# Performance work log

Measured on AMD Instinct MI355X. Metric: run time of the kernel, lower is better.

Reference implementation:

```python
import jax, jax.numpy as jnp
import numpy as np

B, S, D = 2, 2048, 1024
H, DQK, DV = 16, 64, 64
DECAY = 0.85


def _fractal_weights(seq_len: int, decay: float) -> np.ndarray:
    # Dragon-curve hierarchical weights: earlier (coarser) positions get higher
    # weight; weight decays by `decay` per hierarchy level. Normalized to sum 1,
    # matching DragonCurveGenerator.get_hierarchical_weights semantics.
    idx = np.arange(seq_len)
    level = np.floor(np.log2(idx + 1)).astype(np.int32)
    w = decay ** level.astype(np.float32)
    return (w / w.sum()).astype(np.float32)


def setup_inputs() -> dict:
    key = jax.random.key(0)
    kx, kq, kk, kv, ko = jax.random.split(key, 5)
    s = 1.0 / np.sqrt(D)
    return {
        "x": jax.random.normal(kx, (B, S, D), dtype=jnp.float32),
        "Wq": jax.random.normal(kq, (D, H * DQK), dtype=jnp.float32) * s,
        "Wk": jax.random.normal(kk, (D, H * DQK), dtype=jnp.float32) * s,
        "Wv": jax.random.normal(kv, (D, H * DV), dtype=jnp.float32) * s,
        "Wo": jax.random.normal(ko, (H * DV, D), dtype=jnp.float32) * s,
        "fractal_weights": jnp.asarray(_fractal_weights(S, DECAY)),
    }


def reference(x, Wq, Wk, Wv, Wo, fractal_weights):
    b, s, _ = x.shape
    # Projections (Linear with bias=False); weights stored as (in, out).
    Q = (x @ Wq).reshape(b, s, H, DQK).transpose(0, 2, 1, 3)  # [B,H,S,Dqk]
    K = (x @ Wk).reshape(b, s, H, DQK).transpose(0, 2, 1, 3)
    V = (x @ Wv).reshape(b, s, H, DV).transpose(0, 2, 1, 3)   # [B,H,S,Dv]
    scale = 1.0 / jnp.sqrt(jnp.asarray(DQK, dtype=x.dtype))
    scores = jnp.einsum("bhqd,bhkd->bhqk", Q, K) * scale      # [B,H,S,S]
    # Multiplicative per-key fractal bias applied BEFORE softmax.
    scores = scores * fractal_weights[None, None, None, :]
    attn = jax.nn.softmax(scores, axis=-1)
    out = jnp.einsum("bhqk,bhkd->bhqd", attn, V)               # [B,H,S,Dv]
    out = out.transpose(0, 2, 1, 3).reshape(b, s, H * DV)
    return out @ Wo                                            # [B,S,D]
```

## Files before the change

### kernel.cpp

```cpp
#include <hip/hip_runtime.h>
#include <hip/hip_bf16.h>
#include <stdint.h>

#define B_  2
#define S_  2048
#define D_  1024
#define H_  16
#define DH_ 64

typedef __attribute__((ext_vector_type(8))) __bf16    bf16x8;
typedef __attribute__((ext_vector_type(8))) _Float16  f16x8;
typedef __attribute__((ext_vector_type(4))) _Float16  f16x4;
typedef __attribute__((ext_vector_type(2))) __fp16    fp16x2;
typedef __attribute__((ext_vector_type(4))) float     f32x4;

__device__ inline unsigned short f2bf(float f) {
    union { float f; uint32_t u; } v; v.f = f;
    uint32_t r = (v.u + 0x7fffu + ((v.u >> 16) & 1u)) >> 16;
    return (unsigned short)r;
}

__device__ __forceinline__ void g2l16(const unsigned short* g, unsigned short* l) {
    __builtin_amdgcn_global_load_lds(
        (const __attribute__((address_space(1))) unsigned int*)g,
        (__attribute__((address_space(3))) unsigned int*)l,
        16, 0, 0);
}


__global__ void convert_x(const float* __restrict__ x, unsigned short* __restrict__ xb, int n) {
    int i = (blockIdx.x * blockDim.x + threadIdx.x) * 4;
    if (i < n) {
        float4 v = *(const float4*)(x + i);
        ushort4 o;
        o.x = f2bf(v.x); o.y = f2bf(v.y); o.z = f2bf(v.z); o.w = f2bf(v.w);
        *(ushort4*)(xb + i) = o;
    }
}

__global__ void transpose_w(const float* __restrict__ s0, const float* __restrict__ s1,
                            const float* __restrict__ s2, const float* __restrict__ s3,
                            unsigned short* __restrict__ d0, unsigned short* __restrict__ d1,
                            unsigned short* __restrict__ d2, unsigned short* __restrict__ d3) {
    __shared__ float tile[32][33];
    const float* src; unsigned short* dst;
    switch (blockIdx.z) {
        case 0: src = s0; dst = d0; break;
        case 1: src = s1; dst = d1; break;
        case 2: src = s2; dst = d2; break;
        default: src = s3; dst = d3; break;
    }
    int n0 = blockIdx.x * 32, k0 = blockIdx.y * 32;
    int tx = threadIdx.x, ty = threadIdx.y;
    for (int j = 0; j < 32; j += 8)
        tile[ty + j][tx] = src[(long)(k0 + ty + j) * 1024 + n0 + tx];
    __syncthreads();
    for (int j = 0; j < 32; j += 8)
        dst[(long)(n0 + ty + j) * 1024 + k0 + tx] = f2bf(tile[tx][ty + j]);
}

__global__ __launch_bounds__(256, 2)
void gemm128(const unsigned short* __restrict__ A, const unsigned short* __restrict__ Bt,
             unsigned short* __restrict__ Qo, unsigned short* __restrict__ Ko,
             unsigned short* __restrict__ Vt,
             const float* __restrict__ fw)
{
    __shared__ __align__(16) unsigned short As[128 * 64];
    __shared__ __align__(16) unsigned short Bs[128 * 64];
    const int tid  = threadIdx.x;
    const int lane = tid & 63, wid = tid >> 6;
    const int quad = lane >> 4, l15 = lane & 15;
    const int wm = wid >> 1, wn = wid & 1;
    const int bm = blockIdx.y, bn = blockIdx.x;
    const int K = 1024;
    f32x4 acc[4][4] = {};
    const long Abase = (long)bm * 128 * K;
    const long Bbase = (long)bn * 128 * K;

    for (int k0 = 0; k0 < K; k0 += 64) {
        __syncthreads();
#pragma unroll
        for (int i = 0; i < 4; i++) {
            int slot = i * 256 + wid * 64 + lane;
            int row = slot >> 3, cp = slot & 7;
            int c = cp ^ (row & 7);
            g2l16(A + Abase + (long)row * K + k0 + c * 8, &As[(i * 256 + wid * 64) * 8]);
        }
#pragma unroll
        for (int i = 0; i < 4; i++) {
            int slot = i * 256 + wid * 64 + lane;
            int row = slot >> 3, cp = slot & 7;
            int c = cp ^ (row & 7);
            g2l16(Bt + Bbase + (long)row * K + k0 + c * 8, &Bs[(i * 256 + wid * 64) * 8]);
        }
        __syncthreads();
#pragma unroll
        for (int ks = 0; ks < 2; ks++) {
            bf16x8 af[4], bfr[4];
#pragma unroll
            for (int t = 0; t < 4; t++) {
                int ra = wm * 64 + t * 16 + l15;
                af[t]  = *(const bf16x8*)(As + ra * 64 + (((ks * 4 + quad) ^ (l15 & 7))) * 8);
                int rb = wn * 64 + t * 16 + l15;
                bfr[t] = *(const bf16x8*)(Bs + rb * 64 + (((ks * 4 + quad) ^ (l15 & 7))) * 8);
            }
#pragma unroll
            for (int tm = 0; tm < 4; tm++)
#pragma unroll
                for (int tn = 0; tn < 4; tn++)
                    acc[tm][tn] = __builtin_amdgcn_mfma_f32_16x16x32_bf16(af[tm], bfr[tn], acc[tm][tn], 0, 0, 0);
        }
    }

    const float Cq = 0.125f * 1.44269504f;
    for (int tm = 0; tm < 4; tm++)
        for (int tn = 0; tn < 4; tn++)
            for (int r = 0; r < 4; r++) {
                int gm = bm * 128 + wm * 64 + tm * 16 + quad * 4 + r;
                int gn = bn * 128 + wn * 64 + tn * 16 + l15;
                float v = acc[tm][tn][r];
                int b = gm >> 11, s = gm & 2047;
                if (gn < 1024) {
                    int h = gn >> 6, d = gn & 63;
                    Qo[(((long)(b * H_ + h) * S_ + s) << 6) + d] = f2bf(v * Cq);
                } else if (gn < 2048) {
                    int g = gn - 1024; int h = g >> 6, d = g & 63;
                    Ko[(((long)(b * H_ + h) * S_ + s) << 6) + d] = f2bf(v * fw[s]);
                } else {
                    int g = gn - 2048; int h = g >> 6, d = g & 63;
                    union { _Float16 h; unsigned short u; } cv;
                    cv.h = (_Float16)v;
                    int sp = s ^ ((d & 8) ? 4 : 0);
                    Vt[((long)(b * H_ + h) * DH_ + d) * S_ + sp] = cv.u;
                }
            }
}

__global__ __launch_bounds__(256, 4)
void gemm_wo(const unsigned short* __restrict__ A, const unsigned short* __restrict__ Bt,
             float* __restrict__ Cout)
{
    __shared__ __align__(16) unsigned short As[64 * 64];
    __shared__ __align__(16) unsigned short Bs[64 * 64];
    const int tid  = threadIdx.x;
    const int lane = tid & 63, wid = tid >> 6;
    const int quad = lane >> 4, l15 = lane & 15;
    const int bm = blockIdx.y, bn = blockIdx.x;
    const int K = 1024;
    f32x4 acc[4] = {};
    const long Abase = (long)bm * 64 * K;
    const long Bbase = (long)bn * 64 * K;

    for (int k0 = 0; k0 < K; k0 += 64) {
        __syncthreads();
#pragma unroll
        for (int i = 0; i < 2; i++) {
            int base = i * 256 + wid * 64;
            int slot = base + lane;
            int row = slot >> 3, cp = slot & 7;
            int c = cp ^ (row & 7);
            g2l16(A + Abase + (long)row * K + k0 + c * 8, &As[base * 8]);
        }
#pragma unroll
        for (int i = 0; i < 2; i++) {
            int base = i * 256 + wid * 64;
            int slot = base + lane;
            int row = slot >> 3, cp = slot & 7;
            int c = cp ^ (row & 7);
            g2l16(Bt + Bbase + (long)row * K + k0 + c * 8, &Bs[base * 8]);
        }
        __syncthreads();
#pragma unroll
        for (int ks = 0; ks < 2; ks++) {
            bf16x8 af, bfr[4];
            {
                int ra = wid * 16 + l15;
                af = *(const bf16x8*)(As + ra * 64 + (((ks * 4 + quad) ^ (l15 & 7))) * 8);
            }
#pragma unroll
            for (int tt = 0; tt < 4; tt++) {
                int rb = tt * 16 + l15;
                bfr[tt] = *(const bf16x8*)(Bs + rb * 64 + (((ks * 4 + quad) ^ (l15 & 7))) * 8);
            }
#pragma unroll
            for (int tn = 0; tn < 4; tn++)
                acc[tn] = __builtin_amdgcn_mfma_f32_16x16x32_bf16(af, bfr[tn], acc[tn], 0, 0, 0);
        }
    }

    for (int tn = 0; tn < 4; tn++)
        for (int r = 0; r < 4; r++) {
            int gm = bm * 64 + wid * 16 + quad * 4 + r;
            int gn = bn * 64 + tn * 16 + l15;
            Cout[(long)gm * 1024 + gn] = acc[tn][r];
        }
}

__global__ __launch_bounds__(512, 2)
void attn_kernel(const unsigned short* __restrict__ Q, const unsigned short* __restrict__ Kb,
                 const unsigned short* __restrict__ Vt,
                 unsigned short* __restrict__ O)
{
    __shared__ __align__(16) unsigned short smem[2][2][2][64 * 64];

    const int tid  = threadIdx.x;
    const int lane = tid & 63, wid = tid >> 6;
    const int half = wid >> 2, sw = wid & 3;
    const int quad = lane >> 4, l15 = lane & 15;
    const int bh = blockIdx.y;
    const int qt = blockIdx.x;

    const unsigned short* Kg = Kb + (long)bh * S_ * DH_;
    const unsigned short* Vg = Vt + (long)bh * (long)DH_ * S_;

    bf16x8 qf[4][2];
#pragma unroll
    for (int st = 0; st < 4; st++) {
        const unsigned short* Qp = Q + ((long)bh * S_ + qt * 256 + sw * 64 + st * 16 + l15) * DH_ + quad * 8;
        qf[st][0] = *(const bf16x8*)(Qp);
        qf[st][1] = *(const bf16x8*)(Qp + 32);
    }

    auto issue = [&](int buf, int kt) {
#pragma unroll
        for (int i = 0; i < 2; i++) {
            int base = i * 256 + sw * 64;
            int slot = base + lane;
            int row = slot >> 3, cp = slot & 7;
            int c = cp ^ (row & 7);
            g2l16(Kg + ((long)(kt * 64 + row) * 64 + c * 8), &smem[half][buf][0][base * 8]);
        }
#pragma unroll
        for (int i = 0; i < 2; i++) {
            int base = i * 256 + sw * 64;
            int slot = base + lane;
            int row = slot >> 3, cp = slot & 7;
            int c = cp ^ (row & 7);
            g2l16(Vg + ((long)row * S_ + kt * 64 + c * 8), &smem[half][buf][1][base * 8]);
        }
    };

    f32x4 oacc[4][4] = {};
    f32x4 lacc[4] = {};
    const f16x8 vone = {(_Float16)1.f, (_Float16)1.f, (_Float16)1.f, (_Float16)1.f,
                        (_Float16)1.f, (_Float16)1.f, (_Float16)1.f, (_Float16)1.f};

    const int kt0 = half * 16;
    issue(0, kt0);
    __syncthreads();

    const int hf = (((quad & 1) ^ ((l15 >> 3) & 1))) * 4;

    for (int t = 0; t < 16; t++) {
        const int cur = t & 1;
        if (t + 1 < 16) issue(1 - cur, kt0 + t + 1);

        const unsigned short* Kc = &smem[half][cur][0][0];
        const unsigned short* Vc = &smem[half][cur][1][0];

        f32x4 sacc[4][4] = {};
#pragma unroll
        for (int kc = 0; kc < 4; kc++) {
            int row = kc * 16 + l15;
            bf16x8 k0 = *(const bf16x8*)(Kc + (row * 8 + (quad       ^ (l15 & 7))) * 8);
            bf16x8 k1 = *(const bf16x8*)(Kc + (row * 8 + ((4 + quad) ^ (l15 & 7))) * 8);
#pragma unroll
            for (int st = 0; st < 4; st++) {
                sacc[st][kc] = __builtin_amdgcn_mfma_f32_16x16x32_bf16(k0, qf[st][0], sacc[st][kc], 0, 0, 0);
                sacc[st][kc] = __builtin_amdgcn_mfma_f32_16x16x32_bf16(k1, qf[st][1], sacc[st][kc], 0, 0, 0);
            }
        }

        f16x8 vfr[2][4];
#pragma unroll
        for (int c = 0; c < 2; c++)
#pragma unroll
            for (int dt = 0; dt < 4; dt++) {
                int row = dt * 16 + l15;
                int p0 = (c * 4 +     (quad >> 1)) ^ (l15 & 7);
                int p1 = (c * 4 + 2 + (quad >> 1)) ^ (l15 & 7);
                f16x4 v0 = *(const f16x4*)(Vc + row * 64 + p0 * 8 + hf);
                f16x4 v1 = *(const f16x4*)(Vc + row * 64 + p1 * 8 + hf);
                vfr[c][dt] = __builtin_shufflevector(v0, v1, 0, 1, 2, 3, 4, 5, 6, 7);
            }

        f16x8 pk8[4][2];
#pragma unroll
        for (int st = 0; st < 4; st++)
#pragma unroll
            for (int c = 0; c < 2; c++) {
                union { uint4 u; f16x8 v; } pku;
#pragma unroll
                for (int hh = 0; hh < 2; hh++) {
                    float p0 = __builtin_amdgcn_exp2f(sacc[st][2 * c + hh][0]);
                    float p1 = __builtin_amdgcn_exp2f(sacc[st][2 * c + hh][1]);
                    float p2 = __builtin_amdgcn_exp2f(sacc[st][2 * c + hh][2]);
                    float p3 = __builtin_amdgcn_exp2f(sacc[st][2 * c + hh][3]);
                    union { fp16x2 h2; unsigned int u; } a, b;
                    a.h2 = __builtin_amdgcn_cvt_pkrtz(p0, p1);
                    b.h2 = __builtin_amdgcn_cvt_pkrtz(p2, p3);
                    if (hh == 0) { pku.u.x = a.u; pku.u.y = b.u; }
                    else         { pku.u.z = a.u; pku.u.w = b.u; }
                }
                pk8[st][c] = pku.v;
            }

#pragma unroll
        for (int c = 0; c < 2; c++) {
#pragma unroll
            for (int st = 0; st < 4; st++)
                lacc[st] = __builtin_amdgcn_mfma_f32_16x16x32_f16(pk8[st][c], vone, lacc[st], 0, 0, 0);
#pragma unroll
            for (int dt = 0; dt < 4; dt++)
#pragma unroll
                for (int st = 0; st < 4; st++)
                    oacc[st][dt] = __builtin_amdgcn_mfma_f32_16x16x32_f16(pk8[st][c], vfr[c][dt], oacc[st][dt], 0, 0, 0);
        }

        __syncthreads();
    }

    float* ov = (float*)&smem[0][0][0][0];
    float* lv = ov + 128 * 66;
    int b = bh >> 4, h = bh & 15;

#pragma unroll
    for (int p = 0; p < 2; p++) {
        if (half == 1) {
#pragma unroll
            for (int si = 0; si < 2; si++) {
                int st = 2 * p + si;
#pragma unroll
                for (int dt = 0; dt < 4; dt++)
#pragma unroll
                    for (int r = 0; r < 4; r++) {
                        int qr = sw * 32 + si * 16 + quad * 4 + r;
                        ov[qr * 66 + dt * 16 + l15] = oacc[st][dt][r];
                    }
                if (l15 == 0) {
#pragma unroll
                    for (int r = 0; r < 4; r++)
                        lv[sw * 32 + si * 16 + quad * 4 + r] = lacc[st][r];
                }
            }
        }
        __syncthreads();
        if (half == 0) {
#pragma unroll
            for (int si = 0; si < 2; si++) {
                int st = 2 * p + si;
#pragma unroll
                for (int r = 0; r < 4; r++) {
                    int qr = sw * 32 + si * 16 + quad * 4 + r;
                    float inv = 1.0f / (lacc[st][r] + lv[qr]);
                    int srow = qt * 256 + sw * 64 + st * 16 + quad * 4 + r;
#pragma unroll
                    for (int dt = 0; dt < 4; dt++) {
                        float val = oacc[st][dt][r] + ov[qr * 66 + dt * 16 + l15];
                        O[((long)(b * S_ + srow)) * 1024 + h * DH_ + dt * 16 + l15] = f2bf(val * inv);
                    }
                }
            }
        }
        __syncthreads();
    }
}


extern "C" void kernel_launch(void* const* d_in, const int* in_sizes, int n_in,
                              void* d_out, int out_size, void* d_ws, size_t ws_size,
                              hipStream_t stream)
{
    const float* x  = (const float*)d_in[0];
    const float* Wq = (const float*)d_in[1];
    const float* Wk = (const float*)d_in[2];
    const float* Wv = (const float*)d_in[3];
    const float* Wo = (const float*)d_in[4];
    const float* fw = (const float*)d_in[5];
    float* out = (float*)d_out;

    char* ws = (char*)d_ws;
    unsigned short* xb    = (unsigned short*)(ws);
    unsigned short* WqkvT = (unsigned short*)(ws + 8388608);
    unsigned short* WoT   = (unsigned short*)(ws + 14680064);
    unsigned short* Qb    = (unsigned short*)(ws + 16777216);
    unsigned short* Kb    = (unsigned short*)(ws + 25165824);
    unsigned short* Vt    = (unsigned short*)(ws + 33554432);
    unsigned short* Ob    = xb;

    convert_x<<<dim3((B_ * S_ * D_) / 4 / 256), dim3(256), 0, stream>>>(x, xb, B_ * S_ * D_);
    transpose_w<<<dim3(32, 32, 4), dim3(32, 8), 0, stream>>>(
        Wq, Wk, Wv, Wo,
        WqkvT, WqkvT + 1024 * 1024, WqkvT + 2 * 1024 * 1024, WoT);
    gemm128<<<dim3(24, 32), dim3(256), 0, stream>>>(xb, WqkvT, Qb, Kb, Vt, fw);
    attn_kernel<<<dim3(S_ / 256, B_ * H_), dim3(512), 0, stream>>>(Qb, Kb, Vt, Ob);
    gemm_wo<<<dim3(16, 64), dim3(256), 0, stream>>>(Ob, WoT, out);
}
```

Measured before the change: 180.1 us.

## Split QKV GEMM K-loop across 8 waves and fuse prep kernels

The QKV projection GEMM now runs 512 threads per block: two groups of four waves each take one half of every 64-wide K slice, and their partial accumulators are reduced through shared memory in the epilogue before the scatter to Q/K/Vt. This is meant to raise wave-level parallelism and latency hiding in the main GEMM, at the cost of a shared-memory reduction with extra barriers. Separately, the x conversion and the weight transpose are merged into one launch to save kernel launch overhead. Register pressure under the new 512,4 launch bounds could force spills.

```diff
diff --git a/kernel.cpp b/kernel.cpp
--- a/kernel.cpp
+++ b/kernel.cpp
@@ -27,50 +27,55 @@
         16, 0, 0);
 }
 
-
-__global__ void convert_x(const float* __restrict__ x, unsigned short* __restrict__ xb, int n) {
-    int i = (blockIdx.x * blockDim.x + threadIdx.x) * 4;
-    if (i < n) {
+__global__ void prep(const float* __restrict__ x, unsigned short* __restrict__ xb,
+                     const float* __restrict__ s0, const float* __restrict__ s1,
+                     const float* __restrict__ s2, const float* __restrict__ s3,
+                     unsigned short* __restrict__ d0, unsigned short* __restrict__ d1,
+                     unsigned short* __restrict__ d2, unsigned short* __restrict__ d3)
+{
+    __shared__ float tile[32][33];
+    int bid = blockIdx.x, tid = threadIdx.x;
+    if (bid < 4096) {
+        int i = (bid * 256 + tid) * 4;
         float4 v = *(const float4*)(x + i);
         ushort4 o;
         o.x = f2bf(v.x); o.y = f2bf(v.y); o.z = f2bf(v.z); o.w = f2bf(v.w);
         *(ushort4*)(xb + i) = o;
-    }
-}
-
-__global__ void transpose_w(const float* __restrict__ s0, const float* __restrict__ s1,
-                            const float* __restrict__ s2, const float* __restrict__ s3,
-                            unsigned short* __restrict__ d0, unsigned short* __restrict__ d1,
-                            unsigned short* __restrict__ d2, unsigned short* __restrict__ d3) {
-    __shared__ float tile[32][33];
-    const float* src; unsigned short* dst;
-    switch (blockIdx.z) {
-        case 0: src = s0; dst = d0; break;
-        case 1: src = s1; dst = d1; break;
-        case 2: src = s2; dst = d2; break;
-        default: src = s3; dst = d3; break;
-    }
-    int n0 = blockIdx.x * 32, k0 = blockIdx.y * 32;
-    int tx = threadIdx.x, ty = threadIdx.y;
-    for (int j = 0; j < 32; j += 8)
-        tile[ty + j][tx] = src[(long)(k0 + ty + j) * 1024 + n0 + tx];
-    __syncthreads();
-    for (int j = 0; j < 32; j += 8)
-        dst[(long)(n0 + ty + j) * 1024 + k0 + tx] = f2bf(tile[tx][ty + j]);
-}
-
-__global__ __launch_bounds__(256, 2)
+    } else {
+        int tb = bid - 4096;
+        int z = tb >> 10, t = tb & 1023;
+        int bx = t & 31, by = t >> 5;
+        const float* src; unsigned short* dst;
+        switch (z) {
+            case 0: src = s0; dst = d0; break;
+            case 1: src = s1; dst = d1; break;
+            case 2: src = s2; dst = d2; break;
+            default: src = s3; dst = d3; break;
+        }
+        int n0 = bx * 32, k0 = by * 32;
+        int tx = tid & 31, ty = tid >> 5;
+        for (int j = 0; j < 32; j += 8)
+            tile[ty + j][tx] = src[(long)(k0 + ty + j) * 1024 + n0 + tx];
+        __syncthreads();
+        for (int j = 0; j < 32; j += 8)
+            dst[(long)(n0 + ty + j) * 1024 + k0 + tx] = f2bf(tile[tx][ty + j]);
+    }
+}
+
+__global__ __launch_bounds__(512, 4)
 void gemm128(const unsigned short* __restrict__ A, const unsigned short* __restrict__ Bt,
              unsigned short* __restrict__ Qo, unsigned short* __restrict__ Ko,
              unsigned short* __restrict__ Vt,
              const float* __restrict__ fw)
 {
-    __shared__ __align__(16) unsigned short As[128 * 64];
-    __shared__ __align__(16) unsigned short Bs[128 * 64];
+    __shared__ __align__(16) unsigned short Smem[2][128 * 64];
+    unsigned short* As = &Smem[0][0];
+    unsigned short* Bs = &Smem[1][0];
     const int tid  = threadIdx.x;
     const int lane = tid & 63, wid = tid >> 6;
     const int quad = lane >> 4, l15 = lane & 15;
-    const int wm = wid >> 1, wn = wid & 1;
+    const int ks   = wid >> 2;
+    const int wm   = (wid >> 1) & 1, wn = wid & 1;
     const int bm = blockIdx.y, bn = blockIdx.x;
     const int K = 1024;
     f32x4 acc[4][4] = {};
@@ -80,60 +85,79 @@
     for (int k0 = 0; k0 < K; k0 += 64) {
         __syncthreads();
 #pragma unroll
-        for (int i = 0; i < 4; i++) {
-            int slot = i * 256 + wid * 64 + lane;
-            int row = slot >> 3, cp = slot & 7;
-            int c = cp ^ (row & 7);
-            g2l16(A + Abase + (long)row * K + k0 + c * 8, &As[(i * 256 + wid * 64) * 8]);
-        }
-#pragma unroll
-        for (int i = 0; i < 4; i++) {
-            int slot = i * 256 + wid * 64 + lane;
-            int row = slot >> 3, cp = slot & 7;
-            int c = cp ^ (row & 7);
-            g2l16(Bt + Bbase + (long)row * K + k0 + c * 8, &Bs[(i * 256 + wid * 64) * 8]);
-        }
-        __syncthreads();
-#pragma unroll
-        for (int ks = 0; ks < 2; ks++) {
-            bf16x8 af[4], bfr[4];
-#pragma unroll
-            for (int t = 0; t < 4; t++) {
-                int ra = wm * 64 + t * 16 + l15;
-                af[t]  = *(const bf16x8*)(As + ra * 64 + (((ks * 4 + quad) ^ (l15 & 7))) * 8);
-                int rb = wn * 64 + t * 16 + l15;
-                bfr[t] = *(const bf16x8*)(Bs + rb * 64 + (((ks * 4 + quad) ^ (l15 & 7))) * 8);
-            }
-#pragma unroll
-            for (int tm = 0; tm < 4; tm++)
-#pragma unroll
-                for (int tn = 0; tn < 4; tn++)
-                    acc[tm][tn] = __builtin_amdgcn_mfma_f32_16x16x32_bf16(af[tm], bfr[tn], acc[tm][tn], 0, 0, 0);
-        }
-    }
-
+        for (int i = 0; i < 2; i++) {
+            int base = i * 512 + wid * 64;
+            int slot = base + lane;
+            int row = slot >> 3, cp = slot & 7;
+            int c = cp ^ (row & 7);
+            g2l16(A + Abase + (long)row * K + k0 + c * 8, &As[base * 8]);
+        }
+#pragma unroll
+        for (int i = 0; i < 2; i++) {
+            int base = i * 512 + wid * 64;
+            int slot = base + lane;
+            int row = slot >> 3, cp = slot & 7;
+            int c = cp ^ (row & 7);
+            g2l16(Bt + Bbase + (long)row * K + k0 + c * 8, &Bs[base * 8]);
+        }
+        __syncthreads();
+        bf16x8 af[4], bfr[4];
+#pragma unroll
+        for (int t = 0; t < 4; t++) {
+            int ra = wm * 64 + t * 16 + l15;
+            af[t]  = *(const bf16x8*)(As + ra * 64 + (((ks * 4 + quad) ^ (l15 & 7))) * 8);
+            int rb = wn * 64 + t * 16 + l15;
+            bfr[t] = *(const bf16x8*)(Bs + rb * 64 + (((ks * 4 + quad) ^ (l15 & 7))) * 8);
+        }
+#pragma unroll
+        for (int tm = 0; tm < 4; tm++)
+#pragma unroll
+            for (int tn = 0; tn < 4; tn++)
+                acc[tm][tn] = __builtin_amdgcn_mfma_f32_16x16x32_bf16(af[tm], bfr[tn], acc[tm][tn], 0, 0, 0);
+    }
+
+    __syncthreads();
+
+    float* ov = (float*)&Smem[0][0];
+    const int slot = wm * 2 + wn;
     const float Cq = 0.125f * 1.44269504f;
-    for (int tm = 0; tm < 4; tm++)
-        for (int tn = 0; tn < 4; tn++)
-            for (int r = 0; r < 4; r++) {
-                int gm = bm * 128 + wm * 64 + tm * 16 + quad * 4 + r;
-                int gn = bn * 128 + wn * 64 + tn * 16 + l15;
-                float v = acc[tm][tn][r];
-                int b = gm >> 11, s = gm & 2047;
-                if (gn < 1024) {
-                    int h = gn >> 6, d = gn & 63;
-                    Qo[(((long)(b * H_ + h) * S_ + s) << 6) + d] = f2bf(v * Cq);
-                } else if (gn < 2048) {
-                    int g = gn - 1024; int h = g >> 6, d = g & 63;
-                    Ko[(((long)(b * H_ + h) * S_ + s) << 6) + d] = f2bf(v * fw[s]);
-                } else {
-                    int g = gn - 2048; int h = g >> 6, d = g & 63;
-                    union { _Float16 h; unsigned short u; } cv;
-                    cv.h = (_Float16)v;
-                    int sp = s ^ ((d & 8) ? 4 : 0);
-                    Vt[((long)(b * H_ + h) * DH_ + d) * S_ + sp] = cv.u;
+
+#pragma unroll
+    for (int p = 0; p < 4; p++) {
+        if (ks == 1) {
+#pragma unroll
+            for (int tn = 0; tn < 4; tn++)
+#pragma unroll
+                for (int r = 0; r < 4; r++)
+                    ov[((slot * 16) + quad * 4 + r) * 66 + tn * 16 + l15] = acc[p][tn][r];
+        }
+        __syncthreads();
+        if (ks == 0) {
+#pragma unroll
+            for (int tn = 0; tn < 4; tn++)
+#pragma unroll
+                for (int r = 0; r < 4; r++) {
+                    float v = acc[p][tn][r] + ov[((slot * 16) + quad * 4 + r) * 66 + tn * 16 + l15];
+                    int gm = bm * 128 + wm * 64 + p * 16 + quad * 4 + r;
+                    int gn = bn * 128 + wn * 64 + tn * 16 + l15;
+                    int b = gm >> 11, s = gm & 2047;
+                    if (gn < 1024) {
+                        int h = gn >> 6, d = gn & 63;
+                        Qo[(((long)(b * H_ + h) * S_ + s) << 6) + d] = f2bf(v * Cq);
+                    } else if (gn < 2048) {
+                        int g = gn - 1024; int h = g >> 6, d = g & 63;
+                        Ko[(((long)(b * H_ + h) * S_ + s) << 6) + d] = f2bf(v * fw[s]);
+                    } else {
+                        int g = gn - 2048; int h = g >> 6, d = g & 63;
+                        union { _Float16 h; unsigned short u; } cv;
+                        cv.h = (_Float16)v;
+                        int sp = s ^ ((d & 8) ? 4 : 0);
+                        Vt[((long)(b * H_ + h) * DH_ + d) * S_ + sp] = cv.u;
+                    }
                 }
-            }
+        }
+        __syncthreads();
+    }
 }
 
 __global__ __launch_bounds__(256, 4)
@@ -388,11 +412,10 @@
     unsigned short* Vt    = (unsigned short*)(ws + 33554432);
     unsigned short* Ob    = xb;
 
-    convert_x<<<dim3((B_ * S_ * D_) / 4 / 256), dim3(256), 0, stream>>>(x, xb, B_ * S_ * D_);
-    transpose_w<<<dim3(32, 32, 4), dim3(32, 8), 0, stream>>>(
-        Wq, Wk, Wv, Wo,
+    prep<<<dim3(4096 + 4096), dim3(256), 0, stream>>>(
+        x, xb, Wq, Wk, Wv, Wo,
         WqkvT, WqkvT + 1024 * 1024, WqkvT + 2 * 1024 * 1024, WoT);
-    gemm128<<<dim3(24, 32), dim3(256), 0, stream>>>(xb, WqkvT, Qb, Kb, Vt, fw);
+    gemm128<<<dim3(24, 32), dim3(512), 0, stream>>>(xb, WqkvT, Qb, Kb, Vt, fw);
     attn_kernel<<<dim3(S_ / 256, B_ * H_), dim3(512), 0, stream>>>(Qb, Kb, Vt, Ob);
     gemm_wo<<<dim3(16, 64), dim3(256), 0, stream>>>(Ob, WoT, out);
 }
```

Result: no change. 183.4 us (+1.8%).
